# Optimization experiments

Measured on AMD Instinct MI355X. Metric: run time of the kernel, lower is better.

Reference implementation:

```python
import jax, jax.numpy as jnp
import numpy as np

N_TBINS = 1024
K = 64
BETA = 100.0
SIGMA = 10.0
EPS = 1e-8
B = 16384


def _irf_kernel():
    # gaussian_pulse centered at (n-1)//2, circ_shifted: normalized and rolled so peak is at bin 0
    t = jnp.arange(N_TBINS, dtype=jnp.float32)
    mu = (N_TBINS - 1) // 2
    g = jnp.exp(-0.5 * ((t - mu) / SIGMA) ** 2)
    g = g / g.sum()
    return jnp.roll(g, -mu)


def _zero_norm(x, axis):
    xz = x - x.mean(axis=axis, keepdims=True)
    return xz / (jnp.linalg.norm(xz, axis=axis, keepdims=True) + EPS)


def setup_inputs() -> dict:
    key = jax.random.key(0)
    k1, k2, k3, k4, k5 = jax.random.split(key, 5)
    bins = jax.random.randint(k1, (B,), 0, N_TBINS)
    photon_counts = jax.random.uniform(k2, (B,), dtype=jnp.float32) * 1000.0 + 100.0
    sbrs = jax.random.uniform(k3, (B,), dtype=jnp.float32) * 5.0 + 0.1
    learnable_input = jnp.ones((N_TBINS, 1), dtype=jnp.float32)
    bound = float(np.sqrt(6.0 / N_TBINS))  # kaiming_uniform_ on (k, n_tbins, 1)
    cmat_weight = jax.random.uniform(k4, (K, N_TBINS), minval=-bound, maxval=bound, dtype=jnp.float32)
    noise_eps = jax.random.normal(k5, (B, N_TBINS), dtype=jnp.float32)
    return {"bins": bins, "photon_counts": photon_counts, "sbrs": sbrs,
            "learnable_input": learnable_input, "cmat_weight": cmat_weight,
            "noise_eps": noise_eps}


def reference(bins, photon_counts, sbrs, learnable_input, cmat_weight, noise_eps):
    x = jax.nn.relu(learnable_input[:, 0])                      # (n,)
    irf = _irf_kernel()
    irf_input = jnp.fft.irfft(jnp.fft.rfft(x) * jnp.fft.rfft(irf), n=N_TBINS)  # circular conv, (n,)
    amb_per_bin = photon_counts / sbrs / N_TBINS                # (B,)
    scaling = photon_counts / irf_input.sum()                   # (B,)
    shifts = bins % N_TBINS
    # torch.roll(v, s): out[t] = v[(t - s) % n]  -> batched gather instead of python loop
    idx = (jnp.arange(N_TBINS)[None, :] - shifts[:, None]) % N_TBINS  # (B, n)
    shifted = irf_input[idx]                                    # (B, n)
    scaled = shifted * scaling[:, None] + amb_per_bin[:, None]  # (B, n)
    noisy = scaled + jnp.sqrt(scaled) * noise_eps               # reparameterized N(0, sqrt(scaled))
    # Conv1d(in=n_tbins, out=k, ksize=1) on (B, n, 1) == matmul
    out = jnp.einsum('kc,bc->bk', cmat_weight, noisy)           # (B, k)
    input_norm = _zero_norm(out, axis=-1)                       # zero-norm over k
    corr_norm = _zero_norm(cmat_weight, axis=0)                 # (k, n), zero-norm over k
    zncc = jnp.einsum('bk,kn->bn', input_norm, corr_norm)       # (B, n)
    sm = jax.nn.softmax(BETA * zncc, axis=-1)
    pred_depths = jnp.sum(sm * jnp.arange(N_TBINS, dtype=jnp.float32), axis=-1)  # (B,)
    return zncc[..., None], pred_depths
```

## Files before the change

### kernel.cpp

```cpp
#include <hip/hip_runtime.h>
#include <math.h>


#define NT 1024

typedef unsigned short u16;
typedef short bf16x8 __attribute__((ext_vector_type(8)));
typedef float f32x4 __attribute__((ext_vector_type(4)));

__device__ __forceinline__ u16 f2bf(float f) {
  unsigned u = __float_as_uint(f);
  u = u + 0x7FFFu + ((u >> 16) & 1u);
  return (u16)(u >> 16);
}
__device__ __forceinline__ float bf2f(u16 h) {
  return __uint_as_float(((unsigned)h) << 16);
}

__global__ __launch_bounds__(1024) void prelude(const float* __restrict__ learn,
                                                float* __restrict__ irf_input,
                                                float* __restrict__ S) {
  __shared__ float red[NT];
  __shared__ float irf_l[NT];
  __shared__ float x_l[NT];
  int t = threadIdx.x;
  float d = ((float)t - 511.0f) / 10.0f;
  float g = expf(-0.5f * d * d);
  red[t] = g;
  __syncthreads();
  for (int s = 512; s > 0; s >>= 1) {
    if (t < s) red[t] += red[t + s];
    __syncthreads();
  }
  float gsum = red[0];
  irf_l[(t - 511) & (NT - 1)] = g / gsum;
  x_l[t] = fmaxf(learn[t], 0.0f);
  __syncthreads();
  float acc = 0.0f;
  for (int dd = -96; dd <= 96; ++dd)
    acc += irf_l[dd & (NT - 1)] * x_l[(t - dd) & (NT - 1)];
  irf_input[t] = acc;
  red[t] = acc;
  __syncthreads();
  for (int s = 512; s > 0; s >>= 1) {
    if (t < s) red[t] += red[t + s];
    __syncthreads();
  }
  if (t == 0) S[0] = red[0];
}

__global__ __launch_bounds__(256) void corr_init(const float* __restrict__ cmat,
                                                 u16* __restrict__ corrTH,
                                                 u16* __restrict__ corrTL,
                                                 u16* __restrict__ cmatH,
                                                 u16* __restrict__ cmatL) {
  int tid = threadIdx.x;
  {
    int idx = blockIdx.x * 256 + tid;
    float v = cmat[idx];
    u16 h = f2bf(v);
    cmatH[idx] = h;
    cmatL[idx] = f2bf(v - bf2f(h));
  }
  int lane = tid & 63;
  int wv = tid >> 6;
  int n = blockIdx.x * 4 + wv;
  float w = cmat[lane * NT + n];
  float s = w;
#pragma unroll
  for (int off = 32; off > 0; off >>= 1) s += __shfl_xor(s, off);
  float mean = s * (1.0f / 64.0f);
  float dd = w - mean;
  float q = dd * dd;
#pragma unroll
  for (int off = 32; off > 0; off >>= 1) q += __shfl_xor(q, off);
  float val = dd / (sqrtf(q) + 1e-8f);
  u16 h = f2bf(val);
  corrTH[n * 64 + lane] = h;
  corrTL[n * 64 + lane] = f2bf(val - bf2f(h));
}

__global__ __launch_bounds__(256, 4) void fused_main(const int* __restrict__ bins,
                                                     const float* __restrict__ photon,
                                                     const float* __restrict__ sbrs,
                                                     const float* __restrict__ noise,
                                                     const float* __restrict__ irfin,
                                                     const float* __restrict__ Sp,
                                                     const u16* __restrict__ cmatH,
                                                     const u16* __restrict__ cmatL,
                                                     const u16* __restrict__ corrTH,
                                                     const u16* __restrict__ corrTL,
                                                     float* __restrict__ zncc,
                                                     float* __restrict__ pred) {
  __shared__ float irf_s[NT];
  __shared__ float part[4][16][68];
  __shared__ u16 inormH[16 * 64];
  __shared__ u16 inormL[16 * 64];
  __shared__ float red_m[4][16];
  __shared__ float red_e[4][16];
  __shared__ float red_n[4][16];

  int tid = threadIdx.x;
  int lane = tid & 63, w = tid >> 6;
  int row = lane & 15, kg = lane >> 4;
  long b0 = (long)blockIdx.x * 16;
  long b = b0 + row;

  int shift = bins[b] & (NT - 1);
  float ph = photon[b];
  float sb = sbrs[b];

  for (int i = tid; i < NT; i += 256) irf_s[i] = irfin[i];
  __syncthreads();
  float S = Sp[0];
  float scal = ph / S;
  float amb = ph / sb * (1.0f / 1024.0f);
  const float* nrow = noise + b * NT + w * 256;

  f32x4 acc[4];
#pragma unroll
  for (int t = 0; t < 4; ++t) acc[t] = (f32x4){0.f, 0.f, 0.f, 0.f};

#pragma unroll 2
  for (int s = 0; s < 8; ++s) {
    int c = 8 * kg + 32 * s;
    int cabs = w * 256 + c;
    float4 nz0 = *reinterpret_cast<const float4*>(nrow + c);
    float4 nz1 = *reinterpret_cast<const float4*>(nrow + c + 4);
    float nzv[8] = {nz0.x, nz0.y, nz0.z, nz0.w, nz1.x, nz1.y, nz1.z, nz1.w};
    bf16x8 ah, al;
#pragma unroll
    for (int e = 0; e < 8; ++e) {
      float sc = fmaf(irf_s[(cabs + e - shift) & (NT - 1)], scal, amb);
      float v = fmaf(sqrtf(sc), nzv[e], sc);
      u16 h = f2bf(v);
      ah[e] = (short)h;
      al[e] = (short)f2bf(v - bf2f(h));
    }
#pragma unroll
    for (int t = 0; t < 4; ++t) {
      const u16* pH = cmatH + (size_t)(16 * t + row) * NT + cabs;
      const u16* pL = cmatL + (size_t)(16 * t + row) * NT + cabs;
      bf16x8 bh = *reinterpret_cast<const bf16x8*>(pH);
      bf16x8 bl = *reinterpret_cast<const bf16x8*>(pL);
      acc[t] = __builtin_amdgcn_mfma_f32_16x16x32_bf16(al, bh, acc[t], 0, 0, 0);
      acc[t] = __builtin_amdgcn_mfma_f32_16x16x32_bf16(ah, bl, acc[t], 0, 0, 0);
      acc[t] = __builtin_amdgcn_mfma_f32_16x16x32_bf16(ah, bh, acc[t], 0, 0, 0);
    }
  }
#pragma unroll
  for (int t = 0; t < 4; ++t)
#pragma unroll
    for (int q = 0; q < 4; ++q) part[w][4 * kg + q][16 * t + row] = acc[t][q];
  __syncthreads();

#pragma unroll
  for (int rr = 0; rr < 4; ++rr) {
    int r = w * 4 + rr;
    float v = part[0][r][lane] + part[1][r][lane] +
              part[2][r][lane] + part[3][r][lane];
    float s = v;
#pragma unroll
    for (int off = 32; off > 0; off >>= 1) s += __shfl_xor(s, off);
    float mean = s * (1.0f / 64.0f);
    float dd = v - mean;
    float q = dd * dd;
#pragma unroll
    for (int off = 32; off > 0; off >>= 1) q += __shfl_xor(q, off);
    float val = dd / (sqrtf(q) + 1e-8f);
    u16 h = f2bf(val);
    u16 lo = f2bf(val - bf2f(h));
    int boff = (r * 128 + lane * 2) ^ ((r & 7) << 4);
    *reinterpret_cast<u16*>(reinterpret_cast<char*>(inormH) + boff) = h;
    *reinterpret_cast<u16*>(reinterpret_cast<char*>(inormL) + boff) = lo;
  }
  __syncthreads();

  int swz = (row & 7) << 4;
  int a0 = (row * 128 + 16 * kg) ^ swz;
  int a1 = (row * 128 + 64 + 16 * kg) ^ swz;
  bf16x8 a2h0 = *reinterpret_cast<const bf16x8*>(reinterpret_cast<const char*>(inormH) + a0);
  bf16x8 a2h1 = *reinterpret_cast<const bf16x8*>(reinterpret_cast<const char*>(inormH) + a1);
  bf16x8 a2l0 = *reinterpret_cast<const bf16x8*>(reinterpret_cast<const char*>(inormL) + a0);
  bf16x8 a2l1 = *reinterpret_cast<const bf16x8*>(reinterpret_cast<const char*>(inormL) + a1);

  f32x4 acc2[16];
  f32x4 mx = {-INFINITY, -INFINITY, -INFINITY, -INFINITY};
#pragma unroll
  for (int j = 0; j < 16; ++j) {
    int n0 = 256 * w + 16 * j;
    const u16* pH = corrTH + (size_t)(n0 + row) * 64 + 8 * kg;
    const u16* pL = corrTL + (size_t)(n0 + row) * 64 + 8 * kg;
    bf16x8 b0h = *reinterpret_cast<const bf16x8*>(pH);
    bf16x8 b1h = *reinterpret_cast<const bf16x8*>(pH + 32);
    bf16x8 b0l = *reinterpret_cast<const bf16x8*>(pL);
    bf16x8 b1l = *reinterpret_cast<const bf16x8*>(pL + 32);
    f32x4 z = {0.f, 0.f, 0.f, 0.f};
    z = __builtin_amdgcn_mfma_f32_16x16x32_bf16(a2l0, b0h, z, 0, 0, 0);
    z = __builtin_amdgcn_mfma_f32_16x16x32_bf16(a2h0, b0l, z, 0, 0, 0);
    z = __builtin_amdgcn_mfma_f32_16x16x32_bf16(a2h0, b0h, z, 0, 0, 0);
    z = __builtin_amdgcn_mfma_f32_16x16x32_bf16(a2l1, b1h, z, 0, 0, 0);
    z = __builtin_amdgcn_mfma_f32_16x16x32_bf16(a2h1, b1l, z, 0, 0, 0);
    z = __builtin_amdgcn_mfma_f32_16x16x32_bf16(a2h1, b1h, z, 0, 0, 0);
    acc2[j] = z;
#pragma unroll
    for (int q = 0; q < 4; ++q) {
      zncc[(b0 + 4 * kg + q) * NT + n0 + row] = z[q];
      mx[q] = fmaxf(mx[q], z[q]);
    }
  }

#pragma unroll
  for (int q = 0; q < 4; ++q) {
#pragma unroll
    for (int off = 1; off < 16; off <<= 1) mx[q] = fmaxf(mx[q], __shfl_xor(mx[q], off));
  }
  if (row == 0) {
#pragma unroll
    for (int q = 0; q < 4; ++q) red_m[w][4 * kg + q] = mx[q];
  }
  __syncthreads();
  f32x4 rm;
#pragma unroll
  for (int q = 0; q < 4; ++q)
    rm[q] = fmaxf(fmaxf(red_m[0][4 * kg + q], red_m[1][4 * kg + q]),
                  fmaxf(red_m[2][4 * kg + q], red_m[3][4 * kg + q]));

  f32x4 es = {0.f, 0.f, 0.f, 0.f}, ns = es;
#pragma unroll
  for (int j = 0; j < 16; ++j) {
    float nf = (float)(256 * w + 16 * j + row);
#pragma unroll
    for (int q = 0; q < 4; ++q) {
      float e = __expf(100.0f * (acc2[j][q] - rm[q]));
      es[q] += e;
      ns[q] = fmaf(nf, e, ns[q]);
    }
  }
#pragma unroll
  for (int q = 0; q < 4; ++q) {
#pragma unroll
    for (int off = 1; off < 16; off <<= 1) {
      es[q] += __shfl_xor(es[q], off);
      ns[q] += __shfl_xor(ns[q], off);
    }
  }
  if (row == 0) {
#pragma unroll
    for (int q = 0; q < 4; ++q) { red_e[w][4 * kg + q] = es[q]; red_n[w][4 * kg + q] = ns[q]; }
  }
  __syncthreads();
  if (tid < 16) {
    float e = red_e[0][tid] + red_e[1][tid] + red_e[2][tid] + red_e[3][tid];
    float n = red_n[0][tid] + red_n[1][tid] + red_n[2][tid] + red_n[3][tid];
    pred[b0 + tid] = n / e;
  }
}

extern "C" void kernel_launch(void* const* d_in, const int* in_sizes, int n_in,
                              void* d_out, int out_size, void* d_ws, size_t ws_size,
                              hipStream_t stream) {
  const int*   bins   = (const int*)d_in[0];
  const float* photon = (const float*)d_in[1];
  const float* sbrs   = (const float*)d_in[2];
  const float* learn  = (const float*)d_in[3];
  const float* cmat   = (const float*)d_in[4];
  const float* noise  = (const float*)d_in[5];
  float* out = (float*)d_out;
  float* wsf = (float*)d_ws;

  float* irf_input = wsf;
  float* Sslot     = wsf + 1024;
  u16* cmatH  = (u16*)(wsf + 2048);
  u16* cmatL  = cmatH + 65536;
  u16* corrTH = cmatL + 65536;
  u16* corrTL = corrTH + 65536;

  int B = in_sizes[0];
  float* pred = out + (size_t)B * NT;

  hipLaunchKernelGGL(prelude, dim3(1), dim3(1024), 0, stream, learn, irf_input, Sslot);
  hipLaunchKernelGGL(corr_init, dim3(256), dim3(256), 0, stream,
                     cmat, corrTH, corrTL, cmatH, cmatL);
  hipLaunchKernelGGL(fused_main, dim3(B / 16), dim3(256), 0, stream,
                     bins, photon, sbrs, noise, irf_input, Sslot,
                     cmatH, cmatL, corrTH, corrTL, out, pred);
}
```

Before: 190.2 us.

## Double irf buffer in global, use 512-thread blocks, prefetch operands in main kernel

The prelude now writes the IRF convolution twice in a row (plus a small tail) so the fused kernel can read the shifted IRF directly from global memory with a contiguous index. That removes the per-block shared-memory staging and its barrier. The fused kernel doubles to 8 waves per block, each covering half as many channels and output bins. It also software-pipelines the noise, IRF and cmat/corr loads one iteration ahead, and splits the second MFMA chain into two independent accumulators. The cost is more registers under launch_bounds(512,4) and more cross-wave reduction work in shared memory.

```diff
diff --git a/kernel.cpp b/kernel.cpp
--- a/kernel.cpp
+++ b/kernel.cpp
@@ -18,7 +18,7 @@
 }
 
 __global__ __launch_bounds__(1024) void prelude(const float* __restrict__ learn,
-                                                float* __restrict__ irf_input,
+                                                float* __restrict__ irf2,
                                                 float* __restrict__ S) {
   __shared__ float red[NT];
   __shared__ float irf_l[NT];
@@ -39,7 +39,9 @@
   float acc = 0.0f;
   for (int dd = -96; dd <= 96; ++dd)
     acc += irf_l[dd & (NT - 1)] * x_l[(t - dd) & (NT - 1)];
-  irf_input[t] = acc;
+  irf2[t] = acc;
+  irf2[t + 1024] = acc;
+  if (t < 16) irf2[t + 2048] = acc;
   red[t] = acc;
   __syncthreads();
   for (int s = 512; s > 0; s >>= 1) {
@@ -80,11 +82,11 @@
   corrTL[n * 64 + lane] = f2bf(val - bf2f(h));
 }
 
-__global__ __launch_bounds__(256, 4) void fused_main(const int* __restrict__ bins,
+__global__ __launch_bounds__(512, 4) void fused_main(const int* __restrict__ bins,
                                                      const float* __restrict__ photon,
                                                      const float* __restrict__ sbrs,
                                                      const float* __restrict__ noise,
-                                                     const float* __restrict__ irfin,
+                                                     const float* __restrict__ irf2,
                                                      const float* __restrict__ Sp,
                                                      const u16* __restrict__ cmatH,
                                                      const u16* __restrict__ cmatL,
@@ -92,13 +94,12 @@
                                                      const u16* __restrict__ corrTL,
                                                      float* __restrict__ zncc,
                                                      float* __restrict__ pred) {
-  __shared__ float irf_s[NT];
-  __shared__ float part[4][16][68];
+  __shared__ float part[8][16][68];
   __shared__ u16 inormH[16 * 64];
   __shared__ u16 inormL[16 * 64];
-  __shared__ float red_m[4][16];
-  __shared__ float red_e[4][16];
-  __shared__ float red_n[4][16];
+  __shared__ float red_m[8][16];
+  __shared__ float red_e[8][16];
+  __shared__ float red_n[8][16];
 
   int tid = threadIdx.x;
   int lane = tid & 63, w = tid >> 6;
@@ -109,29 +110,45 @@
   int shift = bins[b] & (NT - 1);
   float ph = photon[b];
   float sb = sbrs[b];
-
-  for (int i = tid; i < NT; i += 256) irf_s[i] = irfin[i];
-  __syncthreads();
   float S = Sp[0];
   float scal = ph / S;
   float amb = ph / sb * (1.0f / 1024.0f);
-  const float* nrow = noise + b * NT + w * 256;
+
+  const float* nrow = noise + b * NT + w * 128 + 8 * kg;
+  const float* ir = irf2 + (w * 128 + 8 * kg) - shift + 1024;
 
   f32x4 acc[4];
 #pragma unroll
   for (int t = 0; t < 4; ++t) acc[t] = (f32x4){0.f, 0.f, 0.f, 0.f};
 
-#pragma unroll 2
-  for (int s = 0; s < 8; ++s) {
-    int c = 8 * kg + 32 * s;
-    int cabs = w * 256 + c;
-    float4 nz0 = *reinterpret_cast<const float4*>(nrow + c);
-    float4 nz1 = *reinterpret_cast<const float4*>(nrow + c + 4);
-    float nzv[8] = {nz0.x, nz0.y, nz0.z, nz0.w, nz1.x, nz1.y, nz1.z, nz1.w};
+  float4 nza = *reinterpret_cast<const float4*>(nrow);
+  float4 nzb = *reinterpret_cast<const float4*>(nrow + 4);
+  float iva[8];
+#pragma unroll
+  for (int e = 0; e < 8; ++e) iva[e] = ir[e];
+
+#pragma unroll
+  for (int s = 0; s < 4; ++s) {
+    float4 nza_n, nzb_n;
+    float ivn[8];
+    if (s < 3) {
+      nza_n = *reinterpret_cast<const float4*>(nrow + 32 * (s + 1));
+      nzb_n = *reinterpret_cast<const float4*>(nrow + 32 * (s + 1) + 4);
+#pragma unroll
+      for (int e = 0; e < 8; ++e) ivn[e] = ir[32 * (s + 1) + e];
+    }
+    int cabs = w * 128 + 8 * kg + 32 * s;
+    bf16x8 bh[4], bl[4];
+#pragma unroll
+    for (int t = 0; t < 4; ++t) {
+      bh[t] = *reinterpret_cast<const bf16x8*>(cmatH + (size_t)(16 * t + row) * NT + cabs);
+      bl[t] = *reinterpret_cast<const bf16x8*>(cmatL + (size_t)(16 * t + row) * NT + cabs);
+    }
+    float nzv[8] = {nza.x, nza.y, nza.z, nza.w, nzb.x, nzb.y, nzb.z, nzb.w};
     bf16x8 ah, al;
 #pragma unroll
     for (int e = 0; e < 8; ++e) {
-      float sc = fmaf(irf_s[(cabs + e - shift) & (NT - 1)], scal, amb);
+      float sc = fmaf(iva[e], scal, amb);
       float v = fmaf(sqrtf(sc), nzv[e], sc);
       u16 h = f2bf(v);
       ah[e] = (short)h;
@@ -139,14 +156,13 @@
     }
 #pragma unroll
     for (int t = 0; t < 4; ++t) {
-      const u16* pH = cmatH + (size_t)(16 * t + row) * NT + cabs;
-      const u16* pL = cmatL + (size_t)(16 * t + row) * NT + cabs;
-      bf16x8 bh = *reinterpret_cast<const bf16x8*>(pH);
-      bf16x8 bl = *reinterpret_cast<const bf16x8*>(pL);
-      acc[t] = __builtin_amdgcn_mfma_f32_16x16x32_bf16(al, bh, acc[t], 0, 0, 0);
-      acc[t] = __builtin_amdgcn_mfma_f32_16x16x32_bf16(ah, bl, acc[t], 0, 0, 0);
-      acc[t] = __builtin_amdgcn_mfma_f32_16x16x32_bf16(ah, bh, acc[t], 0, 0, 0);
-    }
+      acc[t] = __builtin_amdgcn_mfma_f32_16x16x32_bf16(al, bh[t], acc[t], 0, 0, 0);
+      acc[t] = __builtin_amdgcn_mfma_f32_16x16x32_bf16(ah, bl[t], acc[t], 0, 0, 0);
+      acc[t] = __builtin_amdgcn_mfma_f32_16x16x32_bf16(ah, bh[t], acc[t], 0, 0, 0);
+    }
+    nza = nza_n; nzb = nzb_n;
+#pragma unroll
+    for (int e = 0; e < 8; ++e) iva[e] = ivn[e];
   }
 #pragma unroll
   for (int t = 0; t < 4; ++t)
@@ -155,10 +171,10 @@
   __syncthreads();
 
 #pragma unroll
-  for (int rr = 0; rr < 4; ++rr) {
-    int r = w * 4 + rr;
-    float v = part[0][r][lane] + part[1][r][lane] +
-              part[2][r][lane] + part[3][r][lane];
+  for (int rr = 0; rr < 2; ++rr) {
+    int r = w * 2 + rr;
+    float v = part[0][r][lane] + part[1][r][lane] + part[2][r][lane] + part[3][r][lane] +
+              part[4][r][lane] + part[5][r][lane] + part[6][r][lane] + part[7][r][lane];
     float s = v;
 #pragma unroll
     for (int off = 32; off > 0; off >>= 1) s += __shfl_xor(s, off);
@@ -184,30 +200,40 @@
   bf16x8 a2l0 = *reinterpret_cast<const bf16x8*>(reinterpret_cast<const char*>(inormL) + a0);
   bf16x8 a2l1 = *reinterpret_cast<const bf16x8*>(reinterpret_cast<const char*>(inormL) + a1);
 
-  f32x4 acc2[16];
+  const u16* pH = corrTH + (size_t)(128 * w + row) * 64 + 8 * kg;
+  const u16* pL = corrTL + (size_t)(128 * w + row) * 64 + 8 * kg;
+
+  f32x4 acc2[8];
   f32x4 mx = {-INFINITY, -INFINITY, -INFINITY, -INFINITY};
-#pragma unroll
-  for (int j = 0; j < 16; ++j) {
-    int n0 = 256 * w + 16 * j;
-    const u16* pH = corrTH + (size_t)(n0 + row) * 64 + 8 * kg;
-    const u16* pL = corrTL + (size_t)(n0 + row) * 64 + 8 * kg;
-    bf16x8 b0h = *reinterpret_cast<const bf16x8*>(pH);
-    bf16x8 b1h = *reinterpret_cast<const bf16x8*>(pH + 32);
-    bf16x8 b0l = *reinterpret_cast<const bf16x8*>(pL);
-    bf16x8 b1l = *reinterpret_cast<const bf16x8*>(pL + 32);
-    f32x4 z = {0.f, 0.f, 0.f, 0.f};
-    z = __builtin_amdgcn_mfma_f32_16x16x32_bf16(a2l0, b0h, z, 0, 0, 0);
-    z = __builtin_amdgcn_mfma_f32_16x16x32_bf16(a2h0, b0l, z, 0, 0, 0);
-    z = __builtin_amdgcn_mfma_f32_16x16x32_bf16(a2h0, b0h, z, 0, 0, 0);
-    z = __builtin_amdgcn_mfma_f32_16x16x32_bf16(a2l1, b1h, z, 0, 0, 0);
-    z = __builtin_amdgcn_mfma_f32_16x16x32_bf16(a2h1, b1l, z, 0, 0, 0);
-    z = __builtin_amdgcn_mfma_f32_16x16x32_bf16(a2h1, b1h, z, 0, 0, 0);
+  bf16x8 b0h = *reinterpret_cast<const bf16x8*>(pH);
+  bf16x8 b1h = *reinterpret_cast<const bf16x8*>(pH + 32);
+  bf16x8 b0l = *reinterpret_cast<const bf16x8*>(pL);
+  bf16x8 b1l = *reinterpret_cast<const bf16x8*>(pL + 32);
+#pragma unroll
+  for (int j = 0; j < 8; ++j) {
+    bf16x8 nb0h, nb1h, nb0l, nb1l;
+    if (j < 7) {
+      nb0h = *reinterpret_cast<const bf16x8*>(pH + (j + 1) * 1024);
+      nb1h = *reinterpret_cast<const bf16x8*>(pH + (j + 1) * 1024 + 32);
+      nb0l = *reinterpret_cast<const bf16x8*>(pL + (j + 1) * 1024);
+      nb1l = *reinterpret_cast<const bf16x8*>(pL + (j + 1) * 1024 + 32);
+    }
+    f32x4 z1 = {0.f, 0.f, 0.f, 0.f}, z2 = z1;
+    z1 = __builtin_amdgcn_mfma_f32_16x16x32_bf16(a2l0, b0h, z1, 0, 0, 0);
+    z2 = __builtin_amdgcn_mfma_f32_16x16x32_bf16(a2h0, b0l, z2, 0, 0, 0);
+    z1 = __builtin_amdgcn_mfma_f32_16x16x32_bf16(a2h0, b0h, z1, 0, 0, 0);
+    z2 = __builtin_amdgcn_mfma_f32_16x16x32_bf16(a2l1, b1h, z2, 0, 0, 0);
+    z1 = __builtin_amdgcn_mfma_f32_16x16x32_bf16(a2h1, b1l, z1, 0, 0, 0);
+    z2 = __builtin_amdgcn_mfma_f32_16x16x32_bf16(a2h1, b1h, z2, 0, 0, 0);
+    f32x4 z = z1 + z2;
     acc2[j] = z;
+    int n0 = 128 * w + 16 * j;
 #pragma unroll
     for (int q = 0; q < 4; ++q) {
       zncc[(b0 + 4 * kg + q) * NT + n0 + row] = z[q];
       mx[q] = fmaxf(mx[q], z[q]);
     }
+    b0h = nb0h; b1h = nb1h; b0l = nb0l; b1l = nb1l;
   }
 
 #pragma unroll
@@ -222,14 +248,17 @@
   __syncthreads();
   f32x4 rm;
 #pragma unroll
-  for (int q = 0; q < 4; ++q)
-    rm[q] = fmaxf(fmaxf(red_m[0][4 * kg + q], red_m[1][4 * kg + q]),
-                  fmaxf(red_m[2][4 * kg + q], red_m[3][4 * kg + q]));
+  for (int q = 0; q < 4; ++q) {
+    float m = red_m[0][4 * kg + q];
+#pragma unroll
+    for (int p = 1; p < 8; ++p) m = fmaxf(m, red_m[p][4 * kg + q]);
+    rm[q] = m;
+  }
 
   f32x4 es = {0.f, 0.f, 0.f, 0.f}, ns = es;
 #pragma unroll
-  for (int j = 0; j < 16; ++j) {
-    float nf = (float)(256 * w + 16 * j + row);
+  for (int j = 0; j < 8; ++j) {
+    float nf = (float)(128 * w + 16 * j + row);
 #pragma unroll
     for (int q = 0; q < 4; ++q) {
       float e = __expf(100.0f * (acc2[j][q] - rm[q]));
@@ -251,8 +280,9 @@
   }
   __syncthreads();
   if (tid < 16) {
-    float e = red_e[0][tid] + red_e[1][tid] + red_e[2][tid] + red_e[3][tid];
-    float n = red_n[0][tid] + red_n[1][tid] + red_n[2][tid] + red_n[3][tid];
+    float e = 0.f, n = 0.f;
+#pragma unroll
+    for (int p = 0; p < 8; ++p) { e += red_e[p][tid]; n += red_n[p][tid]; }
     pred[b0 + tid] = n / e;
   }
 }
@@ -269,9 +299,9 @@
   float* out = (float*)d_out;
   float* wsf = (float*)d_ws;
 
-  float* irf_input = wsf;
-  float* Sslot     = wsf + 1024;
-  u16* cmatH  = (u16*)(wsf + 2048);
+  float* irf2  = wsf;
+  float* Sslot = wsf + 2080;
+  u16* cmatH  = (u16*)(wsf + 2084);
   u16* cmatL  = cmatH + 65536;
   u16* corrTH = cmatL + 65536;
   u16* corrTL = corrTH + 65536;
@@ -279,10 +309,10 @@
   int B = in_sizes[0];
   float* pred = out + (size_t)B * NT;
 
-  hipLaunchKernelGGL(prelude, dim3(1), dim3(1024), 0, stream, learn, irf_input, Sslot);
+  hipLaunchKernelGGL(prelude, dim3(1), dim3(1024), 0, stream, learn, irf2, Sslot);
   hipLaunchKernelGGL(corr_init, dim3(256), dim3(256), 0, stream,
                      cmat, corrTH, corrTL, cmatH, cmatL);
-  hipLaunchKernelGGL(fused_main, dim3(B / 16), dim3(256), 0, stream,
-                     bins, photon, sbrs, noise, irf_input, Sslot,
+  hipLaunchKernelGGL(fused_main, dim3(B / 16), dim3(512), 0, stream,
+                     bins, photon, sbrs, noise, irf2, Sslot,
                      cmatH, cmatL, corrTH, corrTL, out, pred);
 }
```

Result: slower. 204.4 us (+7.5%).

## Process 32 rows per block, reuse cmat fragments, and read duplicated irf from global

Applied to the files above, without the earlier changes.

Each block now handles two 16-row tiles, so every cmatH/cmatL fragment load feeds MFMAs for both tiles, halving weight traffic per row. The irf_input buffer is written twice contiguously (plus padding) so shifted gathers become unmasked contiguous global reads, dropping the shared-memory staging and its barrier. The second GEMM software-prefetches the next corr fragment and splits the accumulation into two chains to add MFMA ILP. Occupancy hint drops from 4 to 2 blocks per CU and register pressure rises.

```diff
diff --git a/kernel.cpp b/kernel.cpp
--- a/kernel.cpp
+++ b/kernel.cpp
@@ -18,7 +18,7 @@
 }
 
 __global__ __launch_bounds__(1024) void prelude(const float* __restrict__ learn,
-                                                float* __restrict__ irf_input,
+                                                float* __restrict__ irf2,
                                                 float* __restrict__ S) {
   __shared__ float red[NT];
   __shared__ float irf_l[NT];
@@ -39,7 +39,9 @@
   float acc = 0.0f;
   for (int dd = -96; dd <= 96; ++dd)
     acc += irf_l[dd & (NT - 1)] * x_l[(t - dd) & (NT - 1)];
-  irf_input[t] = acc;
+  irf2[t] = acc;
+  irf2[t + 1024] = acc;
+  if (t < 16) irf2[t + 2048] = acc;
   red[t] = acc;
   __syncthreads();
   for (int s = 512; s > 0; s >>= 1) {
@@ -80,11 +82,11 @@
   corrTL[n * 64 + lane] = f2bf(val - bf2f(h));
 }
 
-__global__ __launch_bounds__(256, 4) void fused_main(const int* __restrict__ bins,
+__global__ __launch_bounds__(256, 2) void fused_main(const int* __restrict__ bins,
                                                      const float* __restrict__ photon,
                                                      const float* __restrict__ sbrs,
                                                      const float* __restrict__ noise,
-                                                     const float* __restrict__ irfin,
+                                                     const float* __restrict__ irf2,
                                                      const float* __restrict__ Sp,
                                                      const u16* __restrict__ cmatH,
                                                      const u16* __restrict__ cmatL,
@@ -92,10 +94,9 @@
                                                      const u16* __restrict__ corrTL,
                                                      float* __restrict__ zncc,
                                                      float* __restrict__ pred) {
-  __shared__ float irf_s[NT];
-  __shared__ float part[4][16][68];
-  __shared__ u16 inormH[16 * 64];
-  __shared__ u16 inormL[16 * 64];
+  __shared__ float part[4][32][68];
+  __shared__ u16 inormH[32 * 64];
+  __shared__ u16 inormL[32 * 64];
   __shared__ float red_m[4][16];
   __shared__ float red_e[4][16];
   __shared__ float red_n[4][16];
@@ -103,60 +104,84 @@
   int tid = threadIdx.x;
   int lane = tid & 63, w = tid >> 6;
   int row = lane & 15, kg = lane >> 4;
-  long b0 = (long)blockIdx.x * 16;
-  long b = b0 + row;
-
-  int shift = bins[b] & (NT - 1);
-  float ph = photon[b];
-  float sb = sbrs[b];
-
-  for (int i = tid; i < NT; i += 256) irf_s[i] = irfin[i];
-  __syncthreads();
+  long b0 = (long)blockIdx.x * 32;
+  long bA = b0 + row;
+  long bB = b0 + 16 + row;
+
+  int shiftA = bins[bA] & (NT - 1);
+  int shiftB = bins[bB] & (NT - 1);
+  float phA = photon[bA], phB = photon[bB];
+  float sbA = sbrs[bA],  sbB = sbrs[bB];
   float S = Sp[0];
-  float scal = ph / S;
-  float amb = ph / sb * (1.0f / 1024.0f);
-  const float* nrow = noise + b * NT + w * 256;
-
-  f32x4 acc[4];
-#pragma unroll
-  for (int t = 0; t < 4; ++t) acc[t] = (f32x4){0.f, 0.f, 0.f, 0.f};
-
-#pragma unroll 2
+  float scalA = phA / S, scalB = phB / S;
+  float ambA = phA / sbA * (1.0f / 1024.0f);
+  float ambB = phB / sbB * (1.0f / 1024.0f);
+
+  const float* nrowA = noise + bA * NT + w * 256 + 8 * kg;
+  const float* nrowB = noise + bB * NT + w * 256 + 8 * kg;
+  const float* irA = irf2 + (w * 256 + 8 * kg) - shiftA + 1024;
+  const float* irB = irf2 + (w * 256 + 8 * kg) - shiftB + 1024;
+
+  f32x4 acc[2][4];
+#pragma unroll
+  for (int rt = 0; rt < 2; ++rt)
+#pragma unroll
+    for (int t = 0; t < 4; ++t) acc[rt][t] = (f32x4){0.f, 0.f, 0.f, 0.f};
+
+#pragma unroll
   for (int s = 0; s < 8; ++s) {
-    int c = 8 * kg + 32 * s;
-    int cabs = w * 256 + c;
-    float4 nz0 = *reinterpret_cast<const float4*>(nrow + c);
-    float4 nz1 = *reinterpret_cast<const float4*>(nrow + c + 4);
-    float nzv[8] = {nz0.x, nz0.y, nz0.z, nz0.w, nz1.x, nz1.y, nz1.z, nz1.w};
-    bf16x8 ah, al;
+    int cabs = w * 256 + 8 * kg + 32 * s;
+    bf16x8 bh[4], bl[4];
+#pragma unroll
+    for (int t = 0; t < 4; ++t) {
+      bh[t] = *reinterpret_cast<const bf16x8*>(cmatH + (size_t)(16 * t + row) * NT + cabs);
+      bl[t] = *reinterpret_cast<const bf16x8*>(cmatL + (size_t)(16 * t + row) * NT + cabs);
+    }
+    float4 nA0 = *reinterpret_cast<const float4*>(nrowA + 32 * s);
+    float4 nA1 = *reinterpret_cast<const float4*>(nrowA + 32 * s + 4);
+    float4 nB0 = *reinterpret_cast<const float4*>(nrowB + 32 * s);
+    float4 nB1 = *reinterpret_cast<const float4*>(nrowB + 32 * s + 4);
+    float ivA[8], ivB[8];
+#pragma unroll
+    for (int e = 0; e < 8; ++e) { ivA[e] = irA[32 * s + e]; ivB[e] = irB[32 * s + e]; }
+    float nzA[8] = {nA0.x, nA0.y, nA0.z, nA0.w, nA1.x, nA1.y, nA1.z, nA1.w};
+    float nzB[8] = {nB0.x, nB0.y, nB0.z, nB0.w, nB1.x, nB1.y, nB1.z, nB1.w};
+    bf16x8 ahA, alA, ahB, alB;
 #pragma unroll
     for (int e = 0; e < 8; ++e) {
-      float sc = fmaf(irf_s[(cabs + e - shift) & (NT - 1)], scal, amb);
-      float v = fmaf(sqrtf(sc), nzv[e], sc);
-      u16 h = f2bf(v);
-      ah[e] = (short)h;
-      al[e] = (short)f2bf(v - bf2f(h));
+      float scA = fmaf(ivA[e], scalA, ambA);
+      float vA = fmaf(sqrtf(scA), nzA[e], scA);
+      u16 hA = f2bf(vA);
+      ahA[e] = (short)hA;
+      alA[e] = (short)f2bf(vA - bf2f(hA));
+      float scB = fmaf(ivB[e], scalB, ambB);
+      float vB = fmaf(sqrtf(scB), nzB[e], scB);
+      u16 hB = f2bf(vB);
+      ahB[e] = (short)hB;
+      alB[e] = (short)f2bf(vB - bf2f(hB));
     }
 #pragma unroll
     for (int t = 0; t < 4; ++t) {
-      const u16* pH = cmatH + (size_t)(16 * t + row) * NT + cabs;
-      const u16* pL = cmatL + (size_t)(16 * t + row) * NT + cabs;
-      bf16x8 bh = *reinterpret_cast<const bf16x8*>(pH);
-      bf16x8 bl = *reinterpret_cast<const bf16x8*>(pL);
-      acc[t] = __builtin_amdgcn_mfma_f32_16x16x32_bf16(al, bh, acc[t], 0, 0, 0);
-      acc[t] = __builtin_amdgcn_mfma_f32_16x16x32_bf16(ah, bl, acc[t], 0, 0, 0);
-      acc[t] = __builtin_amdgcn_mfma_f32_16x16x32_bf16(ah, bh, acc[t], 0, 0, 0);
-    }
-  }
-#pragma unroll
-  for (int t = 0; t < 4; ++t)
-#pragma unroll
-    for (int q = 0; q < 4; ++q) part[w][4 * kg + q][16 * t + row] = acc[t][q];
-  __syncthreads();
-
-#pragma unroll
-  for (int rr = 0; rr < 4; ++rr) {
-    int r = w * 4 + rr;
+      acc[0][t] = __builtin_amdgcn_mfma_f32_16x16x32_bf16(alA, bh[t], acc[0][t], 0, 0, 0);
+      acc[1][t] = __builtin_amdgcn_mfma_f32_16x16x32_bf16(alB, bh[t], acc[1][t], 0, 0, 0);
+      acc[0][t] = __builtin_amdgcn_mfma_f32_16x16x32_bf16(ahA, bl[t], acc[0][t], 0, 0, 0);
+      acc[1][t] = __builtin_amdgcn_mfma_f32_16x16x32_bf16(ahB, bl[t], acc[1][t], 0, 0, 0);
+      acc[0][t] = __builtin_amdgcn_mfma_f32_16x16x32_bf16(ahA, bh[t], acc[0][t], 0, 0, 0);
+      acc[1][t] = __builtin_amdgcn_mfma_f32_16x16x32_bf16(ahB, bh[t], acc[1][t], 0, 0, 0);
+    }
+  }
+#pragma unroll
+  for (int rt = 0; rt < 2; ++rt)
+#pragma unroll
+    for (int t = 0; t < 4; ++t)
+#pragma unroll
+      for (int q = 0; q < 4; ++q)
+        part[w][rt * 16 + 4 * kg + q][16 * t + row] = acc[rt][t][q];
+  __syncthreads();
+
+#pragma unroll
+  for (int rr = 0; rr < 8; ++rr) {
+    int r = w * 8 + rr;
     float v = part[0][r][lane] + part[1][r][lane] +
               part[2][r][lane] + part[3][r][lane];
     float s = v;
@@ -177,83 +202,96 @@
   __syncthreads();
 
   int swz = (row & 7) << 4;
-  int a0 = (row * 128 + 16 * kg) ^ swz;
-  int a1 = (row * 128 + 64 + 16 * kg) ^ swz;
-  bf16x8 a2h0 = *reinterpret_cast<const bf16x8*>(reinterpret_cast<const char*>(inormH) + a0);
-  bf16x8 a2h1 = *reinterpret_cast<const bf16x8*>(reinterpret_cast<const char*>(inormH) + a1);
-  bf16x8 a2l0 = *reinterpret_cast<const bf16x8*>(reinterpret_cast<const char*>(inormL) + a0);
-  bf16x8 a2l1 = *reinterpret_cast<const bf16x8*>(reinterpret_cast<const char*>(inormL) + a1);
-
-  f32x4 acc2[16];
-  f32x4 mx = {-INFINITY, -INFINITY, -INFINITY, -INFINITY};
-#pragma unroll
-  for (int j = 0; j < 16; ++j) {
-    int n0 = 256 * w + 16 * j;
-    const u16* pH = corrTH + (size_t)(n0 + row) * 64 + 8 * kg;
-    const u16* pL = corrTL + (size_t)(n0 + row) * 64 + 8 * kg;
+  const u16* pH = corrTH + (size_t)(256 * w + row) * 64 + 8 * kg;
+  const u16* pL = corrTL + (size_t)(256 * w + row) * 64 + 8 * kg;
+
+#pragma unroll 1
+  for (int rt = 0; rt < 2; ++rt) {
+    int base = rt * 2048;
+    int a0 = base + ((row * 128 + 16 * kg) ^ swz);
+    int a1 = base + ((row * 128 + 64 + 16 * kg) ^ swz);
+    bf16x8 a2h0 = *reinterpret_cast<const bf16x8*>(reinterpret_cast<const char*>(inormH) + a0);
+    bf16x8 a2h1 = *reinterpret_cast<const bf16x8*>(reinterpret_cast<const char*>(inormH) + a1);
+    bf16x8 a2l0 = *reinterpret_cast<const bf16x8*>(reinterpret_cast<const char*>(inormL) + a0);
+    bf16x8 a2l1 = *reinterpret_cast<const bf16x8*>(reinterpret_cast<const char*>(inormL) + a1);
+
+    f32x4 acc2[16];
+    f32x4 mx = {-INFINITY, -INFINITY, -INFINITY, -INFINITY};
     bf16x8 b0h = *reinterpret_cast<const bf16x8*>(pH);
     bf16x8 b1h = *reinterpret_cast<const bf16x8*>(pH + 32);
     bf16x8 b0l = *reinterpret_cast<const bf16x8*>(pL);
     bf16x8 b1l = *reinterpret_cast<const bf16x8*>(pL + 32);
-    f32x4 z = {0.f, 0.f, 0.f, 0.f};
-    z = __builtin_amdgcn_mfma_f32_16x16x32_bf16(a2l0, b0h, z, 0, 0, 0);
-    z = __builtin_amdgcn_mfma_f32_16x16x32_bf16(a2h0, b0l, z, 0, 0, 0);
-    z = __builtin_amdgcn_mfma_f32_16x16x32_bf16(a2h0, b0h, z, 0, 0, 0);
-    z = __builtin_amdgcn_mfma_f32_16x16x32_bf16(a2l1, b1h, z, 0, 0, 0);
-    z = __builtin_amdgcn_mfma_f32_16x16x32_bf16(a2h1, b1l, z, 0, 0, 0);
-    z = __builtin_amdgcn_mfma_f32_16x16x32_bf16(a2h1, b1h, z, 0, 0, 0);
-    acc2[j] = z;
+#pragma unroll
+    for (int j = 0; j < 16; ++j) {
+      int jn = (j + 1) & 15;
+      bf16x8 nb0h = *reinterpret_cast<const bf16x8*>(pH + jn * 1024);
+      bf16x8 nb1h = *reinterpret_cast<const bf16x8*>(pH + jn * 1024 + 32);
+      bf16x8 nb0l = *reinterpret_cast<const bf16x8*>(pL + jn * 1024);
+      bf16x8 nb1l = *reinterpret_cast<const bf16x8*>(pL + jn * 1024 + 32);
+      f32x4 z1 = {0.f, 0.f, 0.f, 0.f}, z2 = z1;
+      z1 = __builtin_amdgcn_mfma_f32_16x16x32_bf16(a2l0, b0h, z1, 0, 0, 0);
+      z2 = __builtin_amdgcn_mfma_f32_16x16x32_bf16(a2h0, b0l, z2, 0, 0, 0);
+      z1 = __builtin_amdgcn_mfma_f32_16x16x32_bf16(a2h0, b0h, z1, 0, 0, 0);
+      z2 = __builtin_amdgcn_mfma_f32_16x16x32_bf16(a2l1, b1h, z2, 0, 0, 0);
+      z1 = __builtin_amdgcn_mfma_f32_16x16x32_bf16(a2h1, b1l, z1, 0, 0, 0);
+      z2 = __builtin_amdgcn_mfma_f32_16x16x32_bf16(a2h1, b1h, z2, 0, 0, 0);
+      f32x4 z = z1 + z2;
+      acc2[j] = z;
+      int n0 = 256 * w + 16 * j;
+#pragma unroll
+      for (int q = 0; q < 4; ++q) {
+        zncc[(b0 + rt * 16 + 4 * kg + q) * NT + n0 + row] = z[q];
+        mx[q] = fmaxf(mx[q], z[q]);
+      }
+      b0h = nb0h; b1h = nb1h; b0l = nb0l; b1l = nb1l;
+    }
+
 #pragma unroll
     for (int q = 0; q < 4; ++q) {
-      zncc[(b0 + 4 * kg + q) * NT + n0 + row] = z[q];
-      mx[q] = fmaxf(mx[q], z[q]);
-    }
-  }
-
-#pragma unroll
-  for (int q = 0; q < 4; ++q) {
-#pragma unroll
-    for (int off = 1; off < 16; off <<= 1) mx[q] = fmaxf(mx[q], __shfl_xor(mx[q], off));
-  }
-  if (row == 0) {
-#pragma unroll
-    for (int q = 0; q < 4; ++q) red_m[w][4 * kg + q] = mx[q];
-  }
-  __syncthreads();
-  f32x4 rm;
-#pragma unroll
-  for (int q = 0; q < 4; ++q)
-    rm[q] = fmaxf(fmaxf(red_m[0][4 * kg + q], red_m[1][4 * kg + q]),
-                  fmaxf(red_m[2][4 * kg + q], red_m[3][4 * kg + q]));
-
-  f32x4 es = {0.f, 0.f, 0.f, 0.f}, ns = es;
-#pragma unroll
-  for (int j = 0; j < 16; ++j) {
-    float nf = (float)(256 * w + 16 * j + row);
+#pragma unroll
+      for (int off = 1; off < 16; off <<= 1) mx[q] = fmaxf(mx[q], __shfl_xor(mx[q], off));
+    }
+    if (row == 0) {
+#pragma unroll
+      for (int q = 0; q < 4; ++q) red_m[w][4 * kg + q] = mx[q];
+    }
+    __syncthreads();
+    f32x4 rm;
+#pragma unroll
+    for (int q = 0; q < 4; ++q)
+      rm[q] = fmaxf(fmaxf(red_m[0][4 * kg + q], red_m[1][4 * kg + q]),
+                    fmaxf(red_m[2][4 * kg + q], red_m[3][4 * kg + q]));
+
+    f32x4 es = {0.f, 0.f, 0.f, 0.f}, ns = es;
+#pragma unroll
+    for (int j = 0; j < 16; ++j) {
+      float nf = (float)(256 * w + 16 * j + row);
+#pragma unroll
+      for (int q = 0; q < 4; ++q) {
+        float e = __expf(100.0f * (acc2[j][q] - rm[q]));
+        es[q] += e;
+        ns[q] = fmaf(nf, e, ns[q]);
+      }
+    }
 #pragma unroll
     for (int q = 0; q < 4; ++q) {
-      float e = __expf(100.0f * (acc2[j][q] - rm[q]));
-      es[q] += e;
-      ns[q] = fmaf(nf, e, ns[q]);
-    }
-  }
-#pragma unroll
-  for (int q = 0; q < 4; ++q) {
-#pragma unroll
-    for (int off = 1; off < 16; off <<= 1) {
-      es[q] += __shfl_xor(es[q], off);
-      ns[q] += __shfl_xor(ns[q], off);
-    }
-  }
-  if (row == 0) {
-#pragma unroll
-    for (int q = 0; q < 4; ++q) { red_e[w][4 * kg + q] = es[q]; red_n[w][4 * kg + q] = ns[q]; }
-  }
-  __syncthreads();
-  if (tid < 16) {
-    float e = red_e[0][tid] + red_e[1][tid] + red_e[2][tid] + red_e[3][tid];
-    float n = red_n[0][tid] + red_n[1][tid] + red_n[2][tid] + red_n[3][tid];
-    pred[b0 + tid] = n / e;
+#pragma unroll
+      for (int off = 1; off < 16; off <<= 1) {
+        es[q] += __shfl_xor(es[q], off);
+        ns[q] += __shfl_xor(ns[q], off);
+      }
+    }
+    if (row == 0) {
+#pragma unroll
+      for (int q = 0; q < 4; ++q) { red_e[w][4 * kg + q] = es[q]; red_n[w][4 * kg + q] = ns[q]; }
+    }
+    __syncthreads();
+    if (tid < 16) {
+      float e = red_e[0][tid] + red_e[1][tid] + red_e[2][tid] + red_e[3][tid];
+      float n = red_n[0][tid] + red_n[1][tid] + red_n[2][tid] + red_n[3][tid];
+      pred[b0 + rt * 16 + tid] = n / e;
+    }
+    __syncthreads();
   }
 }
 
@@ -269,9 +307,9 @@
   float* out = (float*)d_out;
   float* wsf = (float*)d_ws;
 
-  float* irf_input = wsf;
-  float* Sslot     = wsf + 1024;
-  u16* cmatH  = (u16*)(wsf + 2048);
+  float* irf2  = wsf;
+  float* Sslot = wsf + 2080;
+  u16* cmatH  = (u16*)(wsf + 2084);
   u16* cmatL  = cmatH + 65536;
   u16* corrTH = cmatL + 65536;
   u16* corrTL = corrTH + 65536;
@@ -279,10 +317,10 @@
   int B = in_sizes[0];
   float* pred = out + (size_t)B * NT;
 
-  hipLaunchKernelGGL(prelude, dim3(1), dim3(1024), 0, stream, learn, irf_input, Sslot);
+  hipLaunchKernelGGL(prelude, dim3(1), dim3(1024), 0, stream, learn, irf2, Sslot);
   hipLaunchKernelGGL(corr_init, dim3(256), dim3(256), 0, stream,
                      cmat, corrTH, corrTL, cmatH, cmatL);
-  hipLaunchKernelGGL(fused_main, dim3(B / 16), dim3(256), 0, stream,
-                     bins, photon, sbrs, noise, irf_input, Sslot,
+  hipLaunchKernelGGL(fused_main, dim3(B / 32), dim3(256), 0, stream,
+                     bins, photon, sbrs, noise, irf2, Sslot,
                      cmatH, cmatL, corrTH, corrTL, out, pred);
 }
```

Result: slower. 211.1 us (+11.0%).
